# Kernel optimization log

Hardware: AMD Instinct MI355X
Metric: run time of the kernel (lower is better)

## Reference

```python
import jax, jax.numpy as jnp
import numpy as np

N_EMBD = 256
B, T = 2, 512


def setup_inputs() -> dict:
    key = jax.random.key(0)
    kx, ks, kv = jax.random.split(key, 3)
    x = jax.random.normal(kx, (B, T, N_EMBD), dtype=jnp.float32)
    # init std 0.02 per nn.init.normal_(..., std=0.02); keeps I - scaled well-conditioned
    skew_param = 0.02 * jax.random.normal(ks, (N_EMBD, N_EMBD), dtype=jnp.float32)
    vector = 0.02 * jax.random.normal(kv, (1, N_EMBD), dtype=jnp.float32)
    return {"x": x, "skew_param": skew_param, "vector": vector}


def reference(x, skew_param, vector):
    n = skew_param.shape[0]
    skew = skew_param - skew_param.T                      # (n, n), skew-symmetric
    # scaled[b,t,i,j] = x[b,t,i] * skew[i,j]  -> (B, T, n, n)
    scaled = x[..., :, None] * skew
    eye = jnp.eye(n, dtype=x.dtype)
    # Cayley transform: (I - scaled)^{-1} (I + scaled), batched over (B, T)
    q = jnp.linalg.solve(eye - scaled, eye + scaled)      # (B, T, n, n)
    # (1, n) @ (B, T, n, n) -> (B, T, n) after squeezing the row dim
    out = jnp.einsum('n,btnm->btm', vector[0], q)
    return out
```

## Files before the change

kernel.cpp:

```cpp
#include <hip/hip_runtime.h>
#include <math.h>

#define N 256
#define G 4
#define BLK 1024
#define S1 9
#define S2 7
#define SLS 10
#define SP1 11
#define VS 268
#define UTS 280
#define RIDGE 3e-5f

typedef _Float16 half8v __attribute__((ext_vector_type(8)));
typedef float float4v __attribute__((ext_vector_type(4)));

#define OFF_K     0
#define OFF_UT0   47168
#define OFF_UT1   49408
#define OFF_ZTW   51648
#define OFF_GRAM  55744
#define OFF_L     57680
#define OFF_D     59280
#define ARENA_SZ  59456

#define LD_FRAG(base, t) (*(const half8v*)((base) + (mn & 3) * UTS + 32 * (t) + 8 * mq))

#define MATVEC(basep, dst) do {                                                        \
    float4v acc0 = {0.f, 0.f, 0.f, 0.f};                                               \
    float4v acc1 = {0.f, 0.f, 0.f, 0.f};                                               \
    _Pragma("unroll")                                                                  \
    for (int t = 0; t < 4; ++t) {                                                      \
        acc0 = __builtin_amdgcn_mfma_f32_16x16x32_f16(Shi[t], LD_FRAG(basep, t), acc0, 0, 0, 0);          \
        acc1 = __builtin_amdgcn_mfma_f32_16x16x32_f16(Shi[t + 4], LD_FRAG(basep, t + 4), acc1, 0, 0, 0);  \
    }                                                                                  \
    float4v accs = acc0 + acc1;                                                        \
    if (mn < 4) *(float4v*)(zTw + wv * 64 + mn * 16 + mq * 4) = accs;                  \
    dst = zTw[wv * 64 + g * 16 + coff];                                                \
} while (0)

__global__ __launch_bounds__(BLK, 4) void cayley_v16(const float* __restrict__ x_all,
                                                     const float* __restrict__ P,
                                                     const float* __restrict__ v_in,
                                                     float* __restrict__ out, int batch) {
    __shared__ __align__(16) char arena[ARENA_SZ];
    float* sK      = (float*)(arena + OFF_K);
    _Float16* uT0  = (_Float16*)(arena + OFF_UT0);
    _Float16* uT1  = (_Float16*)(arena + OFF_UT1);
    float* zTw     = (float*)(arena + OFF_ZTW);
    float* sGram   = (float*)(arena + OFF_GRAM);
    float* sL      = (float*)(arena + OFF_L);
    float* sD      = (float*)(arena + OFF_D);

    const int tid = threadIdx.x;
    const int lane = tid & 63, wv = tid >> 6;
    const int mn = lane & 15, mq = lane >> 4;
    const int c = tid >> 2, g = tid & 3;
    const int coff = lane >> 2;
    const int sys = blockIdx.x * G + g;
    const bool alive = sys < batch;

    half8v Shi[8];
    {
        const int r = 16 * wv + mn;
#pragma unroll
        for (int t = 0; t < 8; ++t) {
            const int k0 = 32 * t + 8 * mq;
            float4v pa = *(const float4v*)(P + r * N + k0);
            float4v pb = *(const float4v*)(P + r * N + k0 + 4);
            half8v hi;
            hi[0] = (_Float16)(pa.x - P[(k0 + 0) * N + r]);
            hi[1] = (_Float16)(pa.y - P[(k0 + 1) * N + r]);
            hi[2] = (_Float16)(pa.z - P[(k0 + 2) * N + r]);
            hi[3] = (_Float16)(pa.w - P[(k0 + 3) * N + r]);
            hi[4] = (_Float16)(pb.x - P[(k0 + 4) * N + r]);
            hi[5] = (_Float16)(pb.y - P[(k0 + 5) * N + r]);
            hi[6] = (_Float16)(pb.z - P[(k0 + 6) * N + r]);
            hi[7] = (_Float16)(pb.w - P[(k0 + 7) * N + r]);
            Shi[t] = hi;
        }
    }

    const float x_own = alive ? x_all[sys * N + c] : 0.f;
    const float v_own = v_in[c];
    float wsol = 0.f;

    for (int sw = 0; sw < 2; ++sw) {
        const int s = sw ? S2 : S1;

        float kq;
        if (sw == 0) {
            kq = alive ? v_own : 0.f;
        } else {
            uT1[g * UTS + c] = (_Float16)(x_own * wsol);
            __syncthreads();
            float zm;
            MATVEC(uT1, zm);
            kq = alive ? (v_own - wsol - zm) : 0.f;
        }
        sK[g * VS + c] = kq;
        uT0[g * UTS + c] = (_Float16)(x_own * kq);
        __syncthreads();

        for (int i = 1; i <= s; ++i) {
            float zm;
            if (i & 1) { MATVEC(uT0, zm); } else { MATVEC(uT1, zm); }
            kq = 0.5f * zm;
            sK[(i * G + g) * VS + c] = kq;
            if (i < s) {
                _Float16* dst = (i & 1) ? uT1 : uT0;
                dst[g * UTS + c] = (_Float16)(x_own * kq);
            }
            __syncthreads();
        }

        const int NP = (s + 1) * (s + 2) / 2;
        for (int pp = wv; pp < NP; pp += 16) {
            int i = 0, rem = pp;
            while (rem >= (s + 1 - i)) { rem -= (s + 1 - i); ++i; }
            const int j = i + rem;
            const int gq = lane >> 4, q = lane & 15;
            const float* ka = sK + (i * G + gq) * VS + 16 * q;
            const float* kb = sK + (j * G + gq) * VS + 16 * q;
            float p;
            {
                float4v a0 = *(const float4v*)(ka);
                float4v b0 = *(const float4v*)(kb);
                float4v a1 = *(const float4v*)(ka + 4);
                float4v b1 = *(const float4v*)(kb + 4);
                p = a0.x * b0.x;
                p = fmaf(a0.y, b0.y, p); p = fmaf(a0.z, b0.z, p); p = fmaf(a0.w, b0.w, p);
                p = fmaf(a1.x, b1.x, p); p = fmaf(a1.y, b1.y, p);
                p = fmaf(a1.z, b1.z, p); p = fmaf(a1.w, b1.w, p);
            }
            {
                float4v a0 = *(const float4v*)(ka + 8);
                float4v b0 = *(const float4v*)(kb + 8);
                float4v a1 = *(const float4v*)(ka + 12);
                float4v b1 = *(const float4v*)(kb + 12);
                p = fmaf(a0.x, b0.x, p); p = fmaf(a0.y, b0.y, p);
                p = fmaf(a0.z, b0.z, p); p = fmaf(a0.w, b0.w, p);
                p = fmaf(a1.x, b1.x, p); p = fmaf(a1.y, b1.y, p);
                p = fmaf(a1.z, b1.z, p); p = fmaf(a1.w, b1.w, p);
            }
            p += __shfl_xor(p, 1); p += __shfl_xor(p, 2);
            p += __shfl_xor(p, 4); p += __shfl_xor(p, 8);
            if (q == 0) {
                sGram[(i * SP1 + j) * G + gq] = p;
                if (i != j) sGram[(j * SP1 + i) * G + gq] = p;
            }
        }
        __syncthreads();

        if (wv < 4) {
            const int gq = wv;
            const int rr = lane;
#define GG(i, j) sGram[((i) * SP1 + (j)) * G + gq]
            float invn_r = 0.f;
            if (rr < s) {
                const float Brr = GG(rr, rr) + 4.f * GG(rr, rr + 1)
                                + 4.f * GG(rr + 1, rr + 1);
                invn_r = (Brr > 1e-30f) ? (1.f / sqrtf(Brr)) : 0.f;
            }
            for (int k = 0; k < s; ++k) {
                const float invn_k = __shfl(invn_r, k);
                float a = 0.f;
                if (rr >= k && rr < s) {
                    if (rr == k) {
                        a = 1.f + RIDGE;
                    } else {
                        const float Brk = GG(rr, k) + 2.f * GG(rr, k + 1)
                                        + 2.f * GG(rr + 1, k) + 4.f * GG(rr + 1, k + 1);
                        a = Brk * invn_r * invn_k;
                    }
                    for (int m = 0; m < k; ++m)
                        a = fmaf(-sL[(rr * SLS + m) * G + gq],
                                 sL[(k * SLS + m) * G + gq], a);
                }
                float dk = __shfl(a, k);
                dk = fmaxf(dk, 0.5f * RIDGE);
                const float invd = 1.f / sqrtf(dk);
                if (rr >= k && rr < s) sL[(rr * SLS + k) * G + gq] = a * invd;
            }
            float trr = 0.f, acc = 0.f;
            const float rhs = (rr < s)
                ? (GG(rr, 0) + 2.f * GG(rr + 1, 0)) * invn_r : 0.f;
#undef GG
            for (int k = 0; k < s; ++k) {
                const float Lkk = sL[(k * SLS + k) * G + gq];
                float tk = (Lkk > 1e-20f) ? (rhs - acc) / Lkk : 0.f;
                tk = __shfl(tk, k);
                if (rr == k) trr = tk;
                if (rr > k && rr < s)
                    acc = fmaf(sL[(rr * SLS + k) * G + gq], tk, acc);
            }
            float crr = 0.f;
            acc = 0.f;
            for (int k = s - 1; k >= 0; --k) {
                const float Lkk = sL[(k * SLS + k) * G + gq];
                float ck = (Lkk > 1e-20f) ? (trr - acc) / Lkk : 0.f;
                ck = __shfl(ck, k);
                if (rr == k) crr = ck;
                if (rr < k) acc = fmaf(sL[(k * SLS + rr) * G + gq], ck, acc);
            }
            if (rr < s) sD[rr * G + gq] = crr * invn_r;
        }
        __syncthreads();

        for (int i = 0; i < s; ++i)
            wsol = fmaf(sD[i * G + g], sK[(i * G + g) * VS + c], wsol);
        __syncthreads();
    }

    if (alive) out[sys * N + c] = 2.f * wsol - v_own;
}

extern "C" void kernel_launch(void* const* d_in, const int* in_sizes, int n_in,
                              void* d_out, int out_size, void* d_ws, size_t ws_size,
                              hipStream_t stream) {
    const float* x = (const float*)d_in[0];
    const float* P = (const float*)d_in[1];
    const float* v = (const float*)d_in[2];
    float* out = (float*)d_out;
    const int batch = in_sizes[0] / N;

    const int nblk = (batch + G - 1) / G;
    hipLaunchKernelGGL(cayley_v16, dim3(nblk), dim3(BLK), 0, stream, x, P, v, out, batch);
}
```

Measured before the change: 94.55 us.

## Halve block size, give each wave two row tiles and each thread two columns

The block drops from 1024 to 512 threads. Each wave now keeps 16 fp16 skew fragments in registers and issues four MFMA chains per matvec, covering 32 rows instead of 16. Each thread handles two columns with vectorized float2/half2 loads and stores, and the result staging uses a padded row-major layout. The goal is fewer threads and fewer barrier participants per block at the cost of more register pressure, and launch_bounds is lowered to 2 blocks per CU.

```diff
diff --git a/kernel.cpp b/kernel.cpp
--- a/kernel.cpp
+++ b/kernel.cpp
@@ -3,46 +3,57 @@
 
 #define N 256
 #define G 4
-#define BLK 1024
+#define BLK 512
 #define S1 9
 #define S2 7
 #define SLS 10
 #define SP1 11
 #define VS 268
 #define UTS 280
+#define ZS 260
 #define RIDGE 3e-5f
 
 typedef _Float16 half8v __attribute__((ext_vector_type(8)));
+typedef _Float16 half2v __attribute__((ext_vector_type(2)));
 typedef float float4v __attribute__((ext_vector_type(4)));
+typedef float float2v __attribute__((ext_vector_type(2)));
 
 #define OFF_K     0
 #define OFF_UT0   47168
 #define OFF_UT1   49408
 #define OFF_ZTW   51648
-#define OFF_GRAM  55744
-#define OFF_L     57680
-#define OFF_D     59280
-#define ARENA_SZ  59456
+#define OFF_GRAM  55808
+#define OFF_L     57744
+#define OFF_D     59344
+#define ARENA_SZ  59504
 
 #define LD_FRAG(base, t) (*(const half8v*)((base) + (mn & 3) * UTS + 32 * (t) + 8 * mq))
 
-#define MATVEC(basep, dst) do {                                                        \
-    float4v acc0 = {0.f, 0.f, 0.f, 0.f};                                               \
-    float4v acc1 = {0.f, 0.f, 0.f, 0.f};                                               \
-    _Pragma("unroll")                                                                  \
-    for (int t = 0; t < 4; ++t) {                                                      \
-        acc0 = __builtin_amdgcn_mfma_f32_16x16x32_f16(Shi[t], LD_FRAG(basep, t), acc0, 0, 0, 0);          \
-        acc1 = __builtin_amdgcn_mfma_f32_16x16x32_f16(Shi[t + 4], LD_FRAG(basep, t + 4), acc1, 0, 0, 0);  \
-    }                                                                                  \
-    float4v accs = acc0 + acc1;                                                        \
-    if (mn < 4) *(float4v*)(zTw + wv * 64 + mn * 16 + mq * 4) = accs;                  \
-    dst = zTw[wv * 64 + g * 16 + coff];                                                \
+#define MATVEC(basep, d0, d1) do {                                                          \
+    float4v ma00_ = {0.f,0.f,0.f,0.f}, ma01_ = {0.f,0.f,0.f,0.f};                           \
+    float4v ma10_ = {0.f,0.f,0.f,0.f}, ma11_ = {0.f,0.f,0.f,0.f};                           \
+    _Pragma("unroll")                                                                       \
+    for (int t_ = 0; t_ < 4; ++t_) {                                                        \
+        half8v mb0_ = LD_FRAG(basep, t_);                                                   \
+        half8v mb1_ = LD_FRAG(basep, t_ + 4);                                               \
+        ma00_ = __builtin_amdgcn_mfma_f32_16x16x32_f16(Shi[t_],      mb0_, ma00_, 0, 0, 0); \
+        ma01_ = __builtin_amdgcn_mfma_f32_16x16x32_f16(Shi[t_ + 4],  mb1_, ma01_, 0, 0, 0); \
+        ma10_ = __builtin_amdgcn_mfma_f32_16x16x32_f16(Shi[8 + t_],  mb0_, ma10_, 0, 0, 0); \
+        ma11_ = __builtin_amdgcn_mfma_f32_16x16x32_f16(Shi[12 + t_], mb1_, ma11_, 0, 0, 0); \
+    }                                                                                       \
+    float4v mz0_ = ma00_ + ma01_, mz1_ = ma10_ + ma11_;                                     \
+    if (mn < 4) {                                                                           \
+        *(float4v*)(zTw + mn * ZS + 32 * wv + 4 * mq) = mz0_;                               \
+        *(float4v*)(zTw + mn * ZS + 32 * wv + 16 + 4 * mq) = mz1_;                          \
+    }                                                                                       \
+    float2v mzz_ = *(const float2v*)(zTw + g * ZS + c0);                                    \
+    d0 = mzz_.x; d1 = mzz_.y;                                                               \
 } while (0)
 
-__global__ __launch_bounds__(BLK, 4) void cayley_v16(const float* __restrict__ x_all,
-                                                     const float* __restrict__ P,
-                                                     const float* __restrict__ v_in,
-                                                     float* __restrict__ out, int batch) {
+__global__ __launch_bounds__(BLK, 2) void cayley_v17b(const float* __restrict__ x_all,
+                                                      const float* __restrict__ P,
+                                                      const float* __restrict__ v_in,
+                                                      float* __restrict__ out, int batch) {
     __shared__ __align__(16) char arena[ARENA_SZ];
     float* sK      = (float*)(arena + OFF_K);
     _Float16* uT0  = (_Float16*)(arena + OFF_UT0);
@@ -55,14 +66,15 @@
     const int tid = threadIdx.x;
     const int lane = tid & 63, wv = tid >> 6;
     const int mn = lane & 15, mq = lane >> 4;
-    const int c = tid >> 2, g = tid & 3;
-    const int coff = lane >> 2;
+    const int g = tid & 3;
+    const int c0 = (tid >> 2) * 2;
     const int sys = blockIdx.x * G + g;
     const bool alive = sys < batch;
 
-    half8v Shi[8];
-    {
-        const int r = 16 * wv + mn;
+    half8v Shi[16];
+#pragma unroll
+    for (int p = 0; p < 2; ++p) {
+        const int r = 32 * wv + 16 * p + mn;
 #pragma unroll
         for (int t = 0; t < 8; ++t) {
             const int k0 = 32 * t + 8 * mq;
@@ -77,45 +89,58 @@
             hi[5] = (_Float16)(pb.y - P[(k0 + 5) * N + r]);
             hi[6] = (_Float16)(pb.z - P[(k0 + 6) * N + r]);
             hi[7] = (_Float16)(pb.w - P[(k0 + 7) * N + r]);
-            Shi[t] = hi;
+            Shi[p * 8 + t] = hi;
         }
     }
 
-    const float x_own = alive ? x_all[sys * N + c] : 0.f;
-    const float v_own = v_in[c];
-    float wsol = 0.f;
+    float2v x2 = {0.f, 0.f};
+    if (alive) x2 = *(const float2v*)(x_all + sys * N + c0);
+    const float2v v2 = *(const float2v*)(v_in + c0);
+    float w0 = 0.f, w1 = 0.f;
 
     for (int sw = 0; sw < 2; ++sw) {
         const int s = sw ? S2 : S1;
 
-        float kq;
+        float k0v, k1v;
         if (sw == 0) {
-            kq = alive ? v_own : 0.f;
+            k0v = alive ? v2.x : 0.f;
+            k1v = alive ? v2.y : 0.f;
         } else {
-            uT1[g * UTS + c] = (_Float16)(x_own * wsol);
+            half2v h;
+            h[0] = (_Float16)(x2.x * w0); h[1] = (_Float16)(x2.y * w1);
+            *(half2v*)(uT1 + g * UTS + c0) = h;
             __syncthreads();
-            float zm;
-            MATVEC(uT1, zm);
-            kq = alive ? (v_own - wsol - zm) : 0.f;
-        }
-        sK[g * VS + c] = kq;
-        uT0[g * UTS + c] = (_Float16)(x_own * kq);
+            float z0, z1;
+            MATVEC(uT1, z0, z1);
+            k0v = alive ? (v2.x - w0 - z0) : 0.f;
+            k1v = alive ? (v2.y - w1 - z1) : 0.f;
+        }
+        {
+            float2v k2 = {k0v, k1v};
+            *(float2v*)(sK + g * VS + c0) = k2;
+            half2v h;
+            h[0] = (_Float16)(x2.x * k0v); h[1] = (_Float16)(x2.y * k1v);
+            *(half2v*)(uT0 + g * UTS + c0) = h;
+        }
         __syncthreads();
 
         for (int i = 1; i <= s; ++i) {
-            float zm;
-            if (i & 1) { MATVEC(uT0, zm); } else { MATVEC(uT1, zm); }
-            kq = 0.5f * zm;
-            sK[(i * G + g) * VS + c] = kq;
+            float z0, z1;
+            if (i & 1) { MATVEC(uT0, z0, z1); } else { MATVEC(uT1, z0, z1); }
+            k0v = 0.5f * z0; k1v = 0.5f * z1;
+            float2v k2 = {k0v, k1v};
+            *(float2v*)(sK + (i * G + g) * VS + c0) = k2;
             if (i < s) {
                 _Float16* dst = (i & 1) ? uT1 : uT0;
-                dst[g * UTS + c] = (_Float16)(x_own * kq);
+                half2v h;
+                h[0] = (_Float16)(x2.x * k0v); h[1] = (_Float16)(x2.y * k1v);
+                *(half2v*)(dst + g * UTS + c0) = h;
             }
             __syncthreads();
         }
 
         const int NP = (s + 1) * (s + 2) / 2;
-        for (int pp = wv; pp < NP; pp += 16) {
+        for (int pp = wv; pp < NP; pp += 8) {
             int i = 0, rem = pp;
             while (rem >= (s + 1 - i)) { rem -= (s + 1 - i); ++i; }
             const int j = i + rem;
@@ -207,12 +232,19 @@
         }
         __syncthreads();
 
-        for (int i = 0; i < s; ++i)
-            wsol = fmaf(sD[i * G + g], sK[(i * G + g) * VS + c], wsol);
+        for (int i = 0; i < s; ++i) {
+            const float ci = sD[i * G + g];
+            float2v k2 = *(const float2v*)(sK + (i * G + g) * VS + c0);
+            w0 = fmaf(ci, k2.x, w0);
+            w1 = fmaf(ci, k2.y, w1);
+        }
         __syncthreads();
     }
 
-    if (alive) out[sys * N + c] = 2.f * wsol - v_own;
+    if (alive) {
+        float2v o2 = {2.f * w0 - v2.x, 2.f * w1 - v2.y};
+        *(float2v*)(out + sys * N + c0) = o2;
+    }
 }
 
 extern "C" void kernel_launch(void* const* d_in, const int* in_sizes, int n_in,
@@ -225,5 +257,5 @@
     const int batch = in_sizes[0] / N;
 
     const int nblk = (batch + G - 1) / G;
-    hipLaunchKernelGGL(cayley_v16, dim3(nblk), dim3(BLK), 0, stream, x, P, v, out, batch);
+    hipLaunchKernelGGL(cayley_v17b, dim3(nblk), dim3(BLK), 0, stream, x, P, v, out, batch);
 }
```

Result: no change. 92.89 us (-1.8%).
